# Kernel optimization log

Measured on AMD Instinct MI355X. Metric: run time of the kernel, lower is better.

Reference implementation:

```python
import jax, jax.numpy as jnp
import numpy as np

N_NODES = 100000
N_EDGES = 1600000
D_IN = 128
D_HID = 128
N_CLS = 16
N_GRAPHS = 64


def setup_inputs() -> dict:
    key = jax.random.key(0)
    ks = jax.random.split(key, 12)
    h = jax.random.normal(ks[0], (N_NODES, D_IN), dtype=jnp.float32)
    src = jax.random.randint(ks[1], (N_EDGES,), 0, N_NODES, dtype=jnp.int32)
    dst = jax.random.randint(ks[2], (N_EDGES,), 0, N_NODES, dtype=jnp.int32)
    graph_ids = jnp.sort(jax.random.randint(ks[3], (N_NODES,), 0, N_GRAPHS, dtype=jnp.int32))
    s = 1.0 / np.sqrt(D_IN)
    W1_self = jax.random.uniform(ks[4], (D_IN, D_HID), jnp.float32, -s, s)
    W1_neigh = jax.random.uniform(ks[5], (D_IN, D_HID), jnp.float32, -s, s)
    b1 = jnp.zeros((D_HID,), jnp.float32)
    s2 = 1.0 / np.sqrt(D_HID)
    W2_self = jax.random.uniform(ks[6], (D_HID, D_HID), jnp.float32, -s2, s2)
    W2_neigh = jax.random.uniform(ks[7], (D_HID, D_HID), jnp.float32, -s2, s2)
    b2 = jnp.zeros((D_HID,), jnp.float32)
    Wc = jax.random.uniform(ks[8], (D_HID, N_CLS), jnp.float32, -s2, s2)
    bc = jnp.zeros((N_CLS,), jnp.float32)
    return {"h": h, "src": src, "dst": dst, "graph_ids": graph_ids, "num_graphs": N_GRAPHS,
            "W1_self": W1_self, "W1_neigh": W1_neigh, "b1": b1,
            "W2_self": W2_self, "W2_neigh": W2_neigh, "b2": b2,
            "Wc": Wc, "bc": bc}


def _sage_conv(h, src, dst, W_self, W_neigh, b):
    # DGL SAGEConv 'mean': out = fc_self(h) + fc_neigh(mean of in-neighbor feats) + bias
    n = h.shape[0]
    msg = jnp.take(h, src, axis=0)                               # [E, d] gather
    agg = jax.ops.segment_sum(msg, dst, num_segments=n)          # [N, d] scatter-add
    deg = jax.ops.segment_sum(jnp.ones((src.shape[0],), h.dtype), dst, num_segments=n)
    neigh = agg / jnp.maximum(deg, 1.0)[:, None]                 # mean, zero-degree safe
    return h @ W_self + neigh @ W_neigh + b


def reference(h, src, dst, graph_ids, num_graphs,
              W1_self, W1_neigh, b1, W2_self, W2_neigh, b2, Wc, bc):
    x = jax.nn.relu(_sage_conv(h, src, dst, W1_self, W1_neigh, b1))
    x = _sage_conv(x, src, dst, W2_self, W2_neigh, b2)
    # dgl.mean_nodes: per-graph mean over node features
    gsum = jax.ops.segment_sum(x, graph_ids, num_segments=num_graphs)    # [G, d]
    gcnt = jax.ops.segment_sum(jnp.ones((x.shape[0],), x.dtype), graph_ids, num_segments=num_graphs)
    hg = gsum / jnp.maximum(gcnt, 1.0)[:, None]
    return hg @ Wc + bc                                                  # [G, num_classes]
```

## Files before the change

kernel.cpp:

```cpp
#include <hip/hip_runtime.h>

#define D        128
#define N_GRAPHS 64
#define N_CLS    16
#define LDA      40
#define SLOTS    48
#define CAP      8192

typedef unsigned int   uint;
typedef unsigned short ushort;
typedef __attribute__((ext_vector_type(8))) short short8;
typedef __attribute__((ext_vector_type(4))) float f32x4;

__device__ inline ushort f2b(float f) {
    uint u = __float_as_uint(f);
    u += 0x7fffu + ((u >> 16) & 1u);
    return (ushort)(u >> 16);
}

__device__ __forceinline__ int swz2i(int row, int col) {
    return row * 256 + (col ^ (((row ^ (row >> 3)) & 7) << 3));
}


__global__ __launch_bounds__(256) void k_boot(
    const float* __restrict__ h, ushort* __restrict__ fb,
    const float* __restrict__ Ws, const float* __restrict__ Wn,
    ushort* __restrict__ wT,
    const int* __restrict__ gid, int* __restrict__ gstart,
    const int* __restrict__ src, const int* __restrict__ dst,
    int* __restrict__ bcount, uint* __restrict__ ebuf,
    int* __restrict__ bcount2, uint* __restrict__ ebuf2, int doP2,
    int E, int NB, int N, int t4) {
    __shared__ int hist[512], base[512], lcur[512];
    int bb = blockIdx.x;
    int t  = threadIdx.x;

    if (bb < 256) {
        int per = (E + 255) / 256;
        int e0 = bb * per;
        int e1 = min(e0 + per, E);
        for (int i = t; i < NB; i += 256) { hist[i] = 0; lcur[i] = 0; }
        __syncthreads();
        for (int e = e0 + t; e < e1; e += 256) atomicAdd(&hist[dst[e] >> 8], 1);
        __syncthreads();
        for (int i = t; i < NB; i += 256)
            base[i] = hist[i] ? atomicAdd(&bcount[i], hist[i]) : 0;
        __syncthreads();
        for (int e = e0 + t; e < e1; e += 256) {
            int dd = dst[e];
            int b = dd >> 8;
            int off = atomicAdd(&lcur[b], 1);
            int pos = base[b] + off;
            if (pos < CAP)
                ebuf[(size_t)b * CAP + pos] = ((uint)src[e] << 8) | (uint)(dd & 255);
        }
    } else if (bb < 512) {
        if (!doP2) return;
        int bb2 = bb - 256;
        int per = (E + 255) / 256;
        int e0 = bb2 * per;
        int e1 = min(e0 + per, E);
        for (int i = t; i < NB; i += 256) { hist[i] = 0; lcur[i] = 0; }
        __syncthreads();
        for (int e = e0 + t; e < e1; e += 256) atomicAdd(&hist[src[e] >> 8], 1);
        __syncthreads();
        for (int i = t; i < NB; i += 256)
            base[i] = hist[i] ? atomicAdd(&bcount2[i], hist[i]) : 0;
        __syncthreads();
        for (int e = e0 + t; e < e1; e += 256) {
            int ss = src[e];
            int bk = ss >> 8;
            int off = atomicAdd(&lcur[bk], 1);
            int pos = base[bk] + off;
            if (pos < CAP)
                ebuf2[(size_t)bk * CAP + pos] =
                    ((uint)dst[e] << 8) | (uint)(ss & 255);
        }
    } else if (bb < 640) {
        int i = (bb - 512) * 256 + t;
        int c = i >> 8, k = i & 255;
        float v = (k < 128) ? Ws[k * 128 + c] : Wn[(k - 128) * 128 + c];
        wT[c * 256 + k] = f2b(v);
    } else if (bb == 640) {
        int g = t;
        if (g <= N_GRAPHS) {
            int lo = 0, hi = N;
            while (lo < hi) {
                int mid = (lo + hi) >> 1;
                if (gid[mid] < g) lo = mid + 1; else hi = mid;
            }
            gstart[g] = lo;
        }
    } else {
        int i = (bb - 641) * 256 + t;
        if (i < t4) {
            float4 v = ((const float4*)h)[i];
            ushort4 o;
            o.x = f2b(v.x); o.y = f2b(v.y); o.z = f2b(v.z); o.w = f2b(v.w);
            ((ushort4*)fb)[i] = o;
        }
    }
}


__global__ __launch_bounds__(1024) void k_bucket(
    const uint* __restrict__ ebuf, const int* __restrict__ bcount,
    const int* __restrict__ gid,
    int* __restrict__ csrf, int* __restrict__ deg, float* __restrict__ invdeg,
    uint2* __restrict__ gipack, int N) {
    __shared__ int ldeg[256];
    __shared__ int lcsr[256 * SLOTS];
    int b = blockIdx.x, t = threadIdx.x;
    if (t < 256) ldeg[t] = 0;
    __syncthreads();
    int cnt = bcount[b];
    if (cnt > CAP) cnt = CAP;
    const uint* __restrict__ eb = ebuf + (size_t)b * CAP;
    for (int i = t; i < cnt; i += 1024) {
        uint r = eb[i];
        int dl = r & 255;
        int sl = atomicAdd(&ldeg[dl], 1);
        if (sl < SLOTS) lcsr[dl * SLOTS + sl] = (int)(r >> 8);
    }
    __syncthreads();
    int n0 = b << 8;
    int lim = (N - n0) * SLOTS;
    if (lim > 256 * SLOTS) lim = 256 * SLOTS;
    for (int i = t; i < lim; i += 1024)
        csrf[(size_t)n0 * SLOTS + i] = lcsr[i];
    if (t < 256 && n0 + t < N) {
        int d = ldeg[t];
        deg[n0 + t] = d;
        float iv = 1.0f / (float)(d > 1 ? d : 1);
        invdeg[n0 + t] = iv;
        gipack[n0 + t] = make_uint2((uint)gid[n0 + t], __float_as_uint(iv));
    }
}


__global__ __launch_bounds__(256) void k_aggb(
    const ushort* __restrict__ fb, const int* __restrict__ deg,
    const int* __restrict__ csrf, const float* __restrict__ invdeg,
    ushort* __restrict__ outb, int N) {
    int lane = threadIdx.x & 63;
    int n = blockIdx.x * 4 + (threadIdx.x >> 6);
    if (n >= N) return;
    int d = deg[n];
    if (d > SLOTS) d = SLOTS;
    const int* __restrict__ lst = csrf + (size_t)n * SLOTS;
    int ej = lane >> 4;
    int cg = lane & 15;

    float acc[8];
#pragma unroll
    for (int i = 0; i < 8; i++) acc[i] = 0.f;

    int e = ej;
    for (; e + 4 < d; e += 8) {
        int s0 = lst[e];
        int s1 = lst[e + 4];
        uint4 v0 = *(const uint4*)(fb + (size_t)s0 * D + cg * 8);
        uint4 v1 = *(const uint4*)(fb + (size_t)s1 * D + cg * 8);
        acc[0] += __uint_as_float(v0.x << 16);
        acc[1] += __uint_as_float(v0.x & 0xffff0000u);
        acc[2] += __uint_as_float(v0.y << 16);
        acc[3] += __uint_as_float(v0.y & 0xffff0000u);
        acc[4] += __uint_as_float(v0.z << 16);
        acc[5] += __uint_as_float(v0.z & 0xffff0000u);
        acc[6] += __uint_as_float(v0.w << 16);
        acc[7] += __uint_as_float(v0.w & 0xffff0000u);
        acc[0] += __uint_as_float(v1.x << 16);
        acc[1] += __uint_as_float(v1.x & 0xffff0000u);
        acc[2] += __uint_as_float(v1.y << 16);
        acc[3] += __uint_as_float(v1.y & 0xffff0000u);
        acc[4] += __uint_as_float(v1.z << 16);
        acc[5] += __uint_as_float(v1.z & 0xffff0000u);
        acc[6] += __uint_as_float(v1.w << 16);
        acc[7] += __uint_as_float(v1.w & 0xffff0000u);
    }
    for (; e < d; e += 4) {
        int s = lst[e];
        uint4 v = *(const uint4*)(fb + (size_t)s * D + cg * 8);
        acc[0] += __uint_as_float(v.x << 16);
        acc[1] += __uint_as_float(v.x & 0xffff0000u);
        acc[2] += __uint_as_float(v.y << 16);
        acc[3] += __uint_as_float(v.y & 0xffff0000u);
        acc[4] += __uint_as_float(v.z << 16);
        acc[5] += __uint_as_float(v.z & 0xffff0000u);
        acc[6] += __uint_as_float(v.w << 16);
        acc[7] += __uint_as_float(v.w & 0xffff0000u);
    }
#pragma unroll
    for (int i = 0; i < 8; i++) {
        acc[i] += __shfl_xor(acc[i], 16);
        acc[i] += __shfl_xor(acc[i], 32);
    }
    if (ej == 0) {
        float id = invdeg[n];
        uint4 o;
        o.x = (uint)f2b(acc[0] * id) | ((uint)f2b(acc[1] * id) << 16);
        o.y = (uint)f2b(acc[2] * id) | ((uint)f2b(acc[3] * id) << 16);
        o.z = (uint)f2b(acc[4] * id) | ((uint)f2b(acc[5] * id) << 16);
        o.w = (uint)f2b(acc[6] * id) | ((uint)f2b(acc[7] * id) << 16);
        *(uint4*)(outb + (size_t)n * D + cg * 8) = o;
    }
}

__global__ __launch_bounds__(256) void k_part2s(
    const int* __restrict__ src, const int* __restrict__ dst,
    int* __restrict__ bcount2, uint* __restrict__ ebuf2, int E, int NB) {
    __shared__ int hist[512], base[512], lcur[512];
    int t = threadIdx.x;
    int per = (E + 255) / 256;
    int e0 = blockIdx.x * per;
    int e1 = min(e0 + per, E);
    for (int i = t; i < NB; i += 256) { hist[i] = 0; lcur[i] = 0; }
    __syncthreads();
    for (int e = e0 + t; e < e1; e += 256) atomicAdd(&hist[src[e] >> 8], 1);
    __syncthreads();
    for (int i = t; i < NB; i += 256)
        base[i] = hist[i] ? atomicAdd(&bcount2[i], hist[i]) : 0;
    __syncthreads();
    for (int e = e0 + t; e < e1; e += 256) {
        int ss = src[e];
        int bk = ss >> 8;
        int off = atomicAdd(&lcur[bk], 1);
        int pos = base[bk] + off;
        if (pos < CAP)
            ebuf2[(size_t)bk * CAP + pos] = ((uint)dst[e] << 8) | (uint)(ss & 255);
    }
}


__global__ __launch_bounds__(256, 2) void k_mm1m(
    const ushort* __restrict__ hb, const ushort* __restrict__ nbb,
    const ushort* __restrict__ wT, const float* __restrict__ b,
    ushort* __restrict__ x1b, int N) {
    __shared__ __align__(16) ushort As[128 * LDA];
    __shared__ __align__(16) ushort Bs[128 * LDA];
    int t    = threadIdx.x;
    int w    = t >> 6;
    int lane = t & 63;
    int m    = lane & 15;
    int quad = lane >> 4;
    int n0   = blockIdx.x * 128;

    f32x4 acc[2][8];
#pragma unroll
    for (int rt = 0; rt < 2; rt++)
#pragma unroll
        for (int ct = 0; ct < 8; ct++) acc[rt][ct] = (f32x4){0.f, 0.f, 0.f, 0.f};

#pragma unroll 1
    for (int kc = 0; kc < 8; kc++) {
        int k0 = kc * 32;
        const ushort* __restrict__ A = (k0 < 128) ? hb : nbb;
        int ka = k0 & 127;
        __syncthreads();
#pragma unroll
        for (int i = 0; i < 2; i++) {
            int linear = i * 256 + t;
            int row = linear >> 2;
            int q   = linear & 3;
            int nn = n0 + row;
            uint4 v = make_uint4(0u, 0u, 0u, 0u);
            if (nn < N) v = *(const uint4*)(A + (size_t)nn * D + ka + q * 8);
            *(uint4*)(&As[row * LDA + q * 8]) = v;
        }
#pragma unroll
        for (int i = 0; i < 2; i++) {
            int linear = i * 256 + t;
            int col = linear >> 2;
            int q   = linear & 3;
            uint4 v = *(const uint4*)(wT + (size_t)col * 256 + k0 + q * 8);
            *(uint4*)(&Bs[col * LDA + q * 8]) = v;
        }
        __syncthreads();
        short8 af[2], bf[8];
#pragma unroll
        for (int rt = 0; rt < 2; rt++)
            af[rt] = *(const short8*)(&As[(w * 32 + rt * 16 + m) * LDA + quad * 8]);
#pragma unroll
        for (int ct = 0; ct < 8; ct++)
            bf[ct] = *(const short8*)(&Bs[(ct * 16 + m) * LDA + quad * 8]);
#pragma unroll
        for (int rt = 0; rt < 2; rt++)
#pragma unroll
            for (int ct = 0; ct < 8; ct++)
                acc[rt][ct] = __builtin_amdgcn_mfma_f32_16x16x32_bf16(
                    af[rt], bf[ct], acc[rt][ct], 0, 0, 0);
    }
#pragma unroll
    for (int ct = 0; ct < 8; ct++) {
        float bias = b[ct * 16 + m];
#pragma unroll
        for (int rt = 0; rt < 2; rt++) {
#pragma unroll
            for (int r = 0; r < 4; r++) {
                int n = n0 + w * 32 + rt * 16 + quad * 4 + r;
                if (n < N)
                    x1b[(size_t)n * D + ct * 16 + m] =
                        f2b(fmaxf(acc[rt][ct][r] + bias, 0.f));
            }
        }
    }
}


__global__ __launch_bounds__(1024, 4) void k_wg(
    const uint* __restrict__ ebuf2, const int* __restrict__ bcount2,
    const uint2* __restrict__ gipack,
    const ushort* __restrict__ x1b, const int* __restrict__ gstart,
    float* __restrict__ S1, float* __restrict__ P, int N, int WSB) {
    __shared__ __align__(16) char smem[131072];

    if (blockIdx.x >= WSB) {
        int b2 = blockIdx.x - WSB;
        int g  = b2 >> 1;
        int ch = b2 & 1;
        int r0 = gstart[g], r1 = gstart[g + 1];
        int len = r1 - r0;
        if (len <= 0) return;
        int L = (len + 1) >> 1;
        int a = r0 + ch * L;
        int bnd = min(a + L, r1);
        if (a >= bnd) return;
        int rp = threadIdx.x >> 6;
        int cp = threadIdx.x & 63;
        float ax = 0.f, ay = 0.f;
        const uint* __restrict__ M = (const uint*)x1b;
        for (int n = a + rp; n < bnd; n += 16) {
            uint v = M[(size_t)n * 64 + cp];
            ax += __uint_as_float(v << 16);
            ay += __uint_as_float(v & 0xffff0000u);
        }
        atomicAdd(&S1[g * D + cp * 2], ax);
        atomicAdd(&S1[g * D + cp * 2 + 1], ay);
        return;
    }

    float*  lwcT = (float*)smem;
    ushort* lxT  = (ushort*)smem;
    ushort* lwcb = (ushort*)(smem + 65536);
    ushort* lwlo = (ushort*)(smem + 98304);

    int b = blockIdx.x, t = threadIdx.x;
    int n0 = b << 8;

    for (int i = t; i < 16384; i += 1024) lwcT[i] = 0.f;
    __syncthreads();

    int cnt = bcount2[b];
    if (cnt > CAP) cnt = CAP;
    const uint* __restrict__ eb = ebuf2 + (size_t)b * CAP;
    for (int i = t; i < cnt; i += 1024) {
        uint r = eb[i];
        int dn = (int)(r >> 8);
        int sl = (int)(r & 255u);
        uint2 gi = gipack[dn];
        atomicAdd(&lwcT[gi.x * 256 + sl], __uint_as_float(gi.y));
    }
    __syncthreads();

    for (int i = t; i < 16384; i += 1024) {
        int g = i >> 8, sl = i & 255;
        float v = lwcT[i];
        ushort hi = f2b(v);
        float fhi = __uint_as_float((uint)hi << 16);
        ushort lo = f2b(v - fhi);
        int si = swz2i(g, sl);
        lwcb[si] = hi;
        lwlo[si] = lo;
    }
    __syncthreads();

    const uint4* __restrict__ x4 = (const uint4*)x1b;
#pragma unroll 1
    for (int it = 0; it < 4; ++it) {
        int l = it * 1024 + t;
        int n = l >> 4, q = l & 15;
        uint4 v = make_uint4(0u, 0u, 0u, 0u);
        int nn = n0 + n;
        if (nn < N) v = x4[(size_t)nn * 16 + q];
        int d0 = q * 8;
        lxT[swz2i(d0 + 0, n)] = (ushort)(v.x & 0xffffu);
        lxT[swz2i(d0 + 1, n)] = (ushort)(v.x >> 16);
        lxT[swz2i(d0 + 2, n)] = (ushort)(v.y & 0xffffu);
        lxT[swz2i(d0 + 3, n)] = (ushort)(v.y >> 16);
        lxT[swz2i(d0 + 4, n)] = (ushort)(v.z & 0xffffu);
        lxT[swz2i(d0 + 5, n)] = (ushort)(v.z >> 16);
        lxT[swz2i(d0 + 6, n)] = (ushort)(v.w & 0xffffu);
        lxT[swz2i(d0 + 7, n)] = (ushort)(v.w >> 16);
    }
    __syncthreads();

    int wv = t >> 6, lane = t & 63, m = lane & 15, quad = lane >> 4;
    int s  = wv & 3;
    int hs = wv >> 2;
    f32x4 acc[2];
    acc[0] = (f32x4){0.f, 0.f, 0.f, 0.f};
    acc[1] = (f32x4){0.f, 0.f, 0.f, 0.f};

#pragma unroll 1
    for (int k8 = 0; k8 < 8; ++k8) {
        int kc = k8 * 32 + quad * 8;
        int ar = s * 16 + m;
        short8 ahi = *(const short8*)&lwcb[swz2i(ar, kc)];
        short8 alo = *(const short8*)&lwlo[swz2i(ar, kc)];
#pragma unroll
        for (int d2 = 0; d2 < 2; ++d2) {
            short8 bfr = *(const short8*)&lxT[swz2i(hs * 32 + d2 * 16 + m, kc)];
            acc[d2] = __builtin_amdgcn_mfma_f32_16x16x32_bf16(alo, bfr, acc[d2], 0, 0, 0);
            acc[d2] = __builtin_amdgcn_mfma_f32_16x16x32_bf16(ahi, bfr, acc[d2], 0, 0, 0);
        }
    }
    float* __restrict__ Pb = P + (size_t)b * 8192;
#pragma unroll
    for (int d2 = 0; d2 < 2; ++d2) {
#pragma unroll
        for (int r = 0; r < 4; ++r) {
            int g = s * 16 + quad * 4 + r;
            Pb[g * 128 + hs * 32 + d2 * 16 + m] = acc[d2][r];
        }
    }
}


__global__ __launch_bounds__(256) void k_final(
    const float* __restrict__ S1, const float* __restrict__ P, int NBLK,
    const int* __restrict__ gstart, const float* __restrict__ W2s,
    const float* __restrict__ W2n, const float* __restrict__ b2,
    const float* __restrict__ Wc, const float* __restrict__ bc,
    float* __restrict__ out) {
    __shared__ float s1[D], s2[2][D], hg[D];
    int g = blockIdx.x, t = threadIdx.x;
    int c = t & 127, hh = t >> 7;
    const float* __restrict__ Pg = P + (size_t)g * 128 + c;
    float a0 = 0.f, a1 = 0.f, a2 = 0.f, a3 = 0.f;
    int bb = hh;
    for (; bb + 6 < NBLK; bb += 8) {
        a0 += Pg[(size_t)bb * 8192];
        a1 += Pg[(size_t)(bb + 2) * 8192];
        a2 += Pg[(size_t)(bb + 4) * 8192];
        a3 += Pg[(size_t)(bb + 6) * 8192];
    }
    for (; bb < NBLK; bb += 2) a0 += Pg[(size_t)bb * 8192];
    s2[hh][c] = a0 + a1 + a2 + a3;
    if (hh == 0) s1[c] = S1[g * D + c];
    __syncthreads();
    if (t < 128) s2[0][c] += s2[1][c];
    __syncthreads();
    if (t < 128) {
        float acc = 0.f;
#pragma unroll 8
        for (int k = 0; k < D; k++) {
            acc = fmaf(s1[k], W2s[k * D + c], acc);
            acc = fmaf(s2[0][k], W2n[k * D + c], acc);
        }
        int cnt = gstart[g + 1] - gstart[g];
        hg[c] = (cnt > 0) ? (acc / (float)cnt + b2[c]) : 0.f;
    }
    __syncthreads();
    if (t < N_CLS) {
        float o = bc[t];
        for (int k = 0; k < D; k++) o = fmaf(hg[k], Wc[k * N_CLS + t], o);
        out[g * N_CLS + t] = o;
    }
}


extern "C" void kernel_launch(void* const* d_in, const int* in_sizes, int n_in,
                              void* d_out, int out_size, void* d_ws, size_t ws_size,
                              hipStream_t stream) {
    const float* h   = (const float*)d_in[0];
    const int*   src = (const int*)d_in[1];
    const int*   dst = (const int*)d_in[2];
    const int*   gid = (const int*)d_in[3];
    const float* W1s = (const float*)d_in[5];
    const float* W1n = (const float*)d_in[6];
    const float* b1  = (const float*)d_in[7];
    const float* W2s = (const float*)d_in[8];
    const float* W2n = (const float*)d_in[9];
    const float* b2  = (const float*)d_in[10];
    const float* Wc  = (const float*)d_in[11];
    const float* bc  = (const float*)d_in[12];
    float* out = (float*)d_out;

    const int N = in_sizes[0] / D;
    const int E = in_sizes[1];
    const int NB = (N + 255) >> 8;

    char* w = (char*)d_ws;
    size_t off = 0;
    auto alloc = [&](size_t elems) -> void* {
        void* p = w + off;
        off += elems * 4;
        return p;
    };
    float* S1      = (float*)alloc((size_t)N_GRAPHS * D);
    int*   bcount  = (int*)alloc(512);
    int*   bcount2 = (int*)alloc(512);
    size_t zero_bytes = off;
    int*   deg    = (int*)alloc(N);
    float* invdeg = (float*)alloc(N);
    uint2* gipack = (uint2*)alloc((size_t)N * 2);
    int*   gstart = (int*)alloc(128);
    int*   csrf   = (int*)alloc((size_t)N * SLOTS);
    ushort* fb    = (ushort*)alloc((size_t)N * 64);
    ushort* nbb   = (ushort*)alloc((size_t)N * 64);
    ushort* x1b   = (ushort*)alloc((size_t)N * 64);
    ushort* wT    = (ushort*)alloc(16384);
    uint*  ebuf = (uint*)nbb;
    float* P    = (float*)fb;

    size_t ebuf2_units = (size_t)NB * CAP;
    bool dedicated = (off + ebuf2_units * 4) <= ws_size;
    uint* ebuf2 = dedicated ? (uint*)alloc(ebuf2_units) : (uint*)csrf;

    hipMemsetAsync(d_ws, 0, zero_bytes, stream);

    int t4 = N * 32;
    int CB = (t4 + 255) / 256;
    int MMB = (N + 127) / 128;
    int AB  = (N + 3) / 4;

    k_boot<<<641 + CB, 256, 0, stream>>>(
        h, fb, W1s, W1n, wT, gid, gstart, src, dst,
        bcount, ebuf, bcount2, ebuf2, dedicated ? 1 : 0, E, NB, N, t4);
    k_bucket<<<NB, 1024, 0, stream>>>(ebuf, bcount, gid, csrf, deg, invdeg, gipack, N);
    k_aggb<<<AB, 256, 0, stream>>>(fb, deg, csrf, invdeg, nbb, N);
    if (!dedicated)
        k_part2s<<<256, 256, 0, stream>>>(src, dst, bcount2, ebuf2, E, NB);
    k_mm1m<<<MMB, 256, 0, stream>>>(fb, nbb, wT, b1, x1b, N);
    k_wg<<<NB + 128, 1024, 0, stream>>>(
        ebuf2, bcount2, gipack, x1b, gstart, S1, P, N, NB);
    k_final<<<N_GRAPHS, 256, 0, stream>>>(
        S1, P, NB, gstart, W2s, W2n, b2, Wc, bc, out);
}
```

Baseline: 308.8 us.

## Fuse edge partitions in boot, unroll gather, move graph sums into mm1 epilogue

The two edge-partitioning passes (by dst and by src) now run in the same blocks, so src/dst are read once for both histograms and scatters. The neighbour-gather loop is unrolled to four outstanding loads per lane to raise memory-level parallelism. The per-graph sum of layer-1 activations is computed in the k_mm1m epilogue using shared-memory partials plus global atomics, which removes the extra pass over x1b from k_wg. In exchange, k_boot blocks do more serial work each, and the epilogue adds atomics and branches.

```diff
diff --git a/kernel.cpp b/kernel.cpp
--- a/kernel.cpp
+++ b/kernel.cpp
@@ -21,6 +21,16 @@
 __device__ __forceinline__ int swz2i(int row, int col) {
     return row * 256 + (col ^ (((row ^ (row >> 3)) & 7) << 3));
 }
+
+#define ACC8(v)                                          \
+    acc[0] += __uint_as_float((v).x << 16);              \
+    acc[1] += __uint_as_float((v).x & 0xffff0000u);      \
+    acc[2] += __uint_as_float((v).y << 16);              \
+    acc[3] += __uint_as_float((v).y & 0xffff0000u);      \
+    acc[4] += __uint_as_float((v).z << 16);              \
+    acc[5] += __uint_as_float((v).z & 0xffff0000u);      \
+    acc[6] += __uint_as_float((v).w << 16);              \
+    acc[7] += __uint_as_float((v).w & 0xffff0000u);
 
 
 __global__ __launch_bounds__(256) void k_boot(
@@ -32,7 +42,8 @@
     int* __restrict__ bcount, uint* __restrict__ ebuf,
     int* __restrict__ bcount2, uint* __restrict__ ebuf2, int doP2,
     int E, int NB, int N, int t4) {
-    __shared__ int hist[512], base[512], lcur[512];
+    __shared__ int h1[512], b1s[512], c1[512];
+    __shared__ int h2[512], b2s[512], c2[512];
     int bb = blockIdx.x;
     int t  = threadIdx.x;
 
@@ -40,49 +51,40 @@
         int per = (E + 255) / 256;
         int e0 = bb * per;
         int e1 = min(e0 + per, E);
-        for (int i = t; i < NB; i += 256) { hist[i] = 0; lcur[i] = 0; }
-        __syncthreads();
-        for (int e = e0 + t; e < e1; e += 256) atomicAdd(&hist[dst[e] >> 8], 1);
-        __syncthreads();
-        for (int i = t; i < NB; i += 256)
-            base[i] = hist[i] ? atomicAdd(&bcount[i], hist[i]) : 0;
+        for (int i = t; i < NB; i += 256) {
+            h1[i] = 0; c1[i] = 0; h2[i] = 0; c2[i] = 0;
+        }
         __syncthreads();
         for (int e = e0 + t; e < e1; e += 256) {
-            int dd = dst[e];
-            int b = dd >> 8;
-            int off = atomicAdd(&lcur[b], 1);
-            int pos = base[b] + off;
-            if (pos < CAP)
-                ebuf[(size_t)b * CAP + pos] = ((uint)src[e] << 8) | (uint)(dd & 255);
-        }
-    } else if (bb < 512) {
-        if (!doP2) return;
-        int bb2 = bb - 256;
-        int per = (E + 255) / 256;
-        int e0 = bb2 * per;
-        int e1 = min(e0 + per, E);
-        for (int i = t; i < NB; i += 256) { hist[i] = 0; lcur[i] = 0; }
+            atomicAdd(&h1[dst[e] >> 8], 1);
+            if (doP2) atomicAdd(&h2[src[e] >> 8], 1);
+        }
         __syncthreads();
-        for (int e = e0 + t; e < e1; e += 256) atomicAdd(&hist[src[e] >> 8], 1);
-        __syncthreads();
-        for (int i = t; i < NB; i += 256)
-            base[i] = hist[i] ? atomicAdd(&bcount2[i], hist[i]) : 0;
+        for (int i = t; i < NB; i += 256) {
+            b1s[i] = h1[i] ? atomicAdd(&bcount[i], h1[i]) : 0;
+            if (doP2) b2s[i] = h2[i] ? atomicAdd(&bcount2[i], h2[i]) : 0;
+        }
         __syncthreads();
         for (int e = e0 + t; e < e1; e += 256) {
             int ss = src[e];
-            int bk = ss >> 8;
-            int off = atomicAdd(&lcur[bk], 1);
-            int pos = base[bk] + off;
-            if (pos < CAP)
-                ebuf2[(size_t)bk * CAP + pos] =
-                    ((uint)dst[e] << 8) | (uint)(ss & 255);
-        }
-    } else if (bb < 640) {
-        int i = (bb - 512) * 256 + t;
+            int dd = dst[e];
+            int bk1 = dd >> 8;
+            int p1 = b1s[bk1] + atomicAdd(&c1[bk1], 1);
+            if (p1 < CAP)
+                ebuf[(size_t)bk1 * CAP + p1] = ((uint)ss << 8) | (uint)(dd & 255);
+            if (doP2) {
+                int bk2 = ss >> 8;
+                int p2 = b2s[bk2] + atomicAdd(&c2[bk2], 1);
+                if (p2 < CAP)
+                    ebuf2[(size_t)bk2 * CAP + p2] = ((uint)dd << 8) | (uint)(ss & 255);
+            }
+        }
+    } else if (bb < 384) {
+        int i = (bb - 256) * 256 + t;
         int c = i >> 8, k = i & 255;
         float v = (k < 128) ? Ws[k * 128 + c] : Wn[(k - 128) * 128 + c];
         wT[c * 256 + k] = f2b(v);
-    } else if (bb == 640) {
+    } else if (bb == 384) {
         int g = t;
         if (g <= N_GRAPHS) {
             int lo = 0, hi = N;
@@ -93,7 +95,7 @@
             gstart[g] = lo;
         }
     } else {
-        int i = (bb - 641) * 256 + t;
+        int i = (bb - 385) * 256 + t;
         if (i < t4) {
             float4 v = ((const float4*)h)[i];
             ushort4 o;
@@ -157,39 +159,28 @@
     for (int i = 0; i < 8; i++) acc[i] = 0.f;
 
     int e = ej;
+    for (; e + 12 < d; e += 16) {
+        int s0 = lst[e];
+        int s1 = lst[e + 4];
+        int s2 = lst[e + 8];
+        int s3 = lst[e + 12];
+        uint4 v0 = *(const uint4*)(fb + (size_t)s0 * D + cg * 8);
+        uint4 v1 = *(const uint4*)(fb + (size_t)s1 * D + cg * 8);
+        uint4 v2 = *(const uint4*)(fb + (size_t)s2 * D + cg * 8);
+        uint4 v3 = *(const uint4*)(fb + (size_t)s3 * D + cg * 8);
+        ACC8(v0); ACC8(v1); ACC8(v2); ACC8(v3);
+    }
     for (; e + 4 < d; e += 8) {
         int s0 = lst[e];
         int s1 = lst[e + 4];
         uint4 v0 = *(const uint4*)(fb + (size_t)s0 * D + cg * 8);
         uint4 v1 = *(const uint4*)(fb + (size_t)s1 * D + cg * 8);
-        acc[0] += __uint_as_float(v0.x << 16);
-        acc[1] += __uint_as_float(v0.x & 0xffff0000u);
-        acc[2] += __uint_as_float(v0.y << 16);
-        acc[3] += __uint_as_float(v0.y & 0xffff0000u);
-        acc[4] += __uint_as_float(v0.z << 16);
-        acc[5] += __uint_as_float(v0.z & 0xffff0000u);
-        acc[6] += __uint_as_float(v0.w << 16);
-        acc[7] += __uint_as_float(v0.w & 0xffff0000u);
-        acc[0] += __uint_as_float(v1.x << 16);
-        acc[1] += __uint_as_float(v1.x & 0xffff0000u);
-        acc[2] += __uint_as_float(v1.y << 16);
-        acc[3] += __uint_as_float(v1.y & 0xffff0000u);
-        acc[4] += __uint_as_float(v1.z << 16);
-        acc[5] += __uint_as_float(v1.z & 0xffff0000u);
-        acc[6] += __uint_as_float(v1.w << 16);
-        acc[7] += __uint_as_float(v1.w & 0xffff0000u);
+        ACC8(v0); ACC8(v1);
     }
     for (; e < d; e += 4) {
         int s = lst[e];
         uint4 v = *(const uint4*)(fb + (size_t)s * D + cg * 8);
-        acc[0] += __uint_as_float(v.x << 16);
-        acc[1] += __uint_as_float(v.x & 0xffff0000u);
-        acc[2] += __uint_as_float(v.y << 16);
-        acc[3] += __uint_as_float(v.y & 0xffff0000u);
-        acc[4] += __uint_as_float(v.z << 16);
-        acc[5] += __uint_as_float(v.z & 0xffff0000u);
-        acc[6] += __uint_as_float(v.w << 16);
-        acc[7] += __uint_as_float(v.w & 0xffff0000u);
+        ACC8(v);
     }
 #pragma unroll
     for (int i = 0; i < 8; i++) {
@@ -236,15 +227,20 @@
 __global__ __launch_bounds__(256, 2) void k_mm1m(
     const ushort* __restrict__ hb, const ushort* __restrict__ nbb,
     const ushort* __restrict__ wT, const float* __restrict__ b,
+    const int* __restrict__ gid, float* __restrict__ S1,
     ushort* __restrict__ x1b, int N) {
     __shared__ __align__(16) ushort As[128 * LDA];
     __shared__ __align__(16) ushort Bs[128 * LDA];
+    __shared__ float s1l[2][128];
     int t    = threadIdx.x;
     int w    = t >> 6;
     int lane = t & 63;
     int m    = lane & 15;
     int quad = lane >> 4;
     int n0   = blockIdx.x * 128;
+
+    ((float*)s1l)[t] = 0.f;
+    if (t < 256) ((float*)s1l)[t + 256 < 512 ? t + 256 : t] = 0.f;
 
     f32x4 acc[2][8];
 #pragma unroll
@@ -291,19 +287,47 @@
                 acc[rt][ct] = __builtin_amdgcn_mfma_f32_16x16x32_bf16(
                     af[rt], bf[ct], acc[rt][ct], 0, 0, 0);
     }
+
+    int g0 = gid[n0];
+    int gofs[2][4];
+#pragma unroll
+    for (int rt = 0; rt < 2; rt++)
+#pragma unroll
+        for (int r = 0; r < 4; r++) {
+            int n = n0 + w * 32 + rt * 16 + quad * 4 + r;
+            gofs[rt][r] = (n < N) ? (gid[n] - g0) : -1;
+        }
+
 #pragma unroll
     for (int ct = 0; ct < 8; ct++) {
         float bias = b[ct * 16 + m];
+        float vlo = 0.f, vhi = 0.f;
 #pragma unroll
         for (int rt = 0; rt < 2; rt++) {
 #pragma unroll
             for (int r = 0; r < 4; r++) {
+                int go = gofs[rt][r];
+                if (go < 0) continue;
                 int n = n0 + w * 32 + rt * 16 + quad * 4 + r;
-                if (n < N)
-                    x1b[(size_t)n * D + ct * 16 + m] =
-                        f2b(fmaxf(acc[rt][ct][r] + bias, 0.f));
+                float v = fmaxf(acc[rt][ct][r] + bias, 0.f);
+                x1b[(size_t)n * D + ct * 16 + m] = f2b(v);
+                if (go == 0) vlo += v;
+                else if (go == 1) vhi += v;
+                else atomicAdd(&S1[(g0 + go) * D + ct * 16 + m], v);
             }
         }
+        vlo += __shfl_xor(vlo, 16); vlo += __shfl_xor(vlo, 32);
+        vhi += __shfl_xor(vhi, 16); vhi += __shfl_xor(vhi, 32);
+        if (quad == 0) {
+            if (vlo != 0.f) atomicAdd(&s1l[0][ct * 16 + m], vlo);
+            if (vhi != 0.f) atomicAdd(&s1l[1][ct * 16 + m], vhi);
+        }
+    }
+    __syncthreads();
+    if (t < 256) {
+        int g = t >> 7, c = t & 127;
+        float v = s1l[g][c];
+        if (v != 0.f && g0 + g < N_GRAPHS) atomicAdd(&S1[(g0 + g) * D + c], v);
     }
 }
 
@@ -311,35 +335,8 @@
 __global__ __launch_bounds__(1024, 4) void k_wg(
     const uint* __restrict__ ebuf2, const int* __restrict__ bcount2,
     const uint2* __restrict__ gipack,
-    const ushort* __restrict__ x1b, const int* __restrict__ gstart,
-    float* __restrict__ S1, float* __restrict__ P, int N, int WSB) {
+    const ushort* __restrict__ x1b, float* __restrict__ P, int N) {
     __shared__ __align__(16) char smem[131072];
-
-    if (blockIdx.x >= WSB) {
-        int b2 = blockIdx.x - WSB;
-        int g  = b2 >> 1;
-        int ch = b2 & 1;
-        int r0 = gstart[g], r1 = gstart[g + 1];
-        int len = r1 - r0;
-        if (len <= 0) return;
-        int L = (len + 1) >> 1;
-        int a = r0 + ch * L;
-        int bnd = min(a + L, r1);
-        if (a >= bnd) return;
-        int rp = threadIdx.x >> 6;
-        int cp = threadIdx.x & 63;
-        float ax = 0.f, ay = 0.f;
-        const uint* __restrict__ M = (const uint*)x1b;
-        for (int n = a + rp; n < bnd; n += 16) {
-            uint v = M[(size_t)n * 64 + cp];
-            ax += __uint_as_float(v << 16);
-            ay += __uint_as_float(v & 0xffff0000u);
-        }
-        atomicAdd(&S1[g * D + cp * 2], ax);
-        atomicAdd(&S1[g * D + cp * 2 + 1], ay);
-        return;
-    }
-
     float*  lwcT = (float*)smem;
     ushort* lxT  = (ushort*)smem;
     ushort* lwcb = (ushort*)(smem + 65536);
@@ -525,16 +522,15 @@
     int MMB = (N + 127) / 128;
     int AB  = (N + 3) / 4;
 
-    k_boot<<<641 + CB, 256, 0, stream>>>(
+    k_boot<<<385 + CB, 256, 0, stream>>>(
         h, fb, W1s, W1n, wT, gid, gstart, src, dst,
         bcount, ebuf, bcount2, ebuf2, dedicated ? 1 : 0, E, NB, N, t4);
     k_bucket<<<NB, 1024, 0, stream>>>(ebuf, bcount, gid, csrf, deg, invdeg, gipack, N);
     k_aggb<<<AB, 256, 0, stream>>>(fb, deg, csrf, invdeg, nbb, N);
     if (!dedicated)
         k_part2s<<<256, 256, 0, stream>>>(src, dst, bcount2, ebuf2, E, NB);
-    k_mm1m<<<MMB, 256, 0, stream>>>(fb, nbb, wT, b1, x1b, N);
-    k_wg<<<NB + 128, 1024, 0, stream>>>(
-        ebuf2, bcount2, gipack, x1b, gstart, S1, P, N, NB);
+    k_mm1m<<<MMB, 256, 0, stream>>>(fb, nbb, wT, b1, gid, S1, x1b, N);
+    k_wg<<<NB, 1024, 0, stream>>>(ebuf2, bcount2, gipack, x1b, P, N);
     k_final<<<N_GRAPHS, 256, 0, stream>>>(
         S1, P, NB, gstart, W2s, W2n, b2, Wc, bc, out);
 }
```

New measurement: 315.1 us. 2.0% more time.
